# Kernel tuning notes

Hardware: AMD Instinct MI355X
Metric: run time of the kernel (lower is better)

## Reference

```python
import jax, jax.numpy as jnp
import numpy as np

DIM = 768
NUM_HEADS = 12
HEAD_DIM = DIM // NUM_HEADS
SCALE = HEAD_DIM ** -0.5


def setup_inputs() -> dict:
    key = jax.random.key(0)
    ks = jax.random.split(key, 9)
    B, L, C = 4, 1024, DIM
    x = jax.random.normal(ks[0], (B, L, C), jnp.float32)
    q_ape = jax.random.normal(ks[1], (1, L, C), jnp.float32)
    k_ape = jax.random.normal(ks[2], (1, L, C), jnp.float32)
    attn_pos = jax.random.normal(ks[3], (1, NUM_HEADS, L, L), jnp.float32)
    s = C ** -0.5
    # torch Linear weights: (out_features, in_features)
    Wq = jax.random.normal(ks[4], (C, C), jnp.float32) * s
    Wk = jax.random.normal(ks[5], (C, C), jnp.float32) * s
    Wv = jax.random.normal(ks[6], (C, C), jnp.float32) * s
    Wp = jax.random.normal(ks[7], (C, C), jnp.float32) * s
    bp = jax.random.normal(ks[8], (C,), jnp.float32) * 0.01
    return {"x": x, "q_ape": q_ape, "k_ape": k_ape, "attn_pos": attn_pos,
            "Wq": Wq, "Wk": Wk, "Wv": Wv, "Wp": Wp, "bp": bp}


def _split_heads(t):
    # (B, L, C) -> (B, H, L, D)
    B, L, C = t.shape
    return t.reshape(B, L, NUM_HEADS, HEAD_DIM).transpose(0, 2, 1, 3)


def reference(x, q_ape, k_ape, attn_pos, Wq, Wk, Wv, Wp, bp):
    B, L, C = x.shape
    q = _split_heads((x + q_ape) @ Wq.T)          # (B,H,L,D)
    k = _split_heads((x + k_ape) @ Wk.T)          # (B,H,L,D)
    v = _split_heads(x @ Wv.T)                    # (B,H,L,D)
    attn = jnp.einsum('bhqd,bhkd->bhqk', q, k) * SCALE + attn_pos
    attn = jax.nn.softmax(attn, axis=-1)
    out = jnp.einsum('bhqk,bhkd->bhqd', attn, v)  # (B,H,L,D)
    out = out.transpose(0, 2, 1, 3).reshape(B, L, C)
    return out @ Wp.T + bp
```

## Files before the change

kernel.cpp:

```cpp
#include <hip/hip_runtime.h>
#include <stdint.h>

#define NH 12
#define HD 64
#define NB 4
#define SEQ 1024
#define CDIM 768
#define MTOT (NB*SEQ)
#define MC   (MTOT*CDIM)
#define LC   (SEQ*CDIM)
#define WSZ  (CDIM*CDIM)
#define ATT_SCALE 0.125f

typedef __attribute__((ext_vector_type(4))) float f32x4;
typedef __attribute__((ext_vector_type(8))) __bf16 bf16x8;
typedef __attribute__((ext_vector_type(8))) short short8;
typedef __attribute__((ext_vector_type(4))) unsigned short ushort4v;
typedef unsigned short u16;

static __device__ __forceinline__ f32x4 mfma16(short8 a, short8 b, f32x4 c) {
  return __builtin_amdgcn_mfma_f32_16x16x32_bf16(
      __builtin_bit_cast(bf16x8, a), __builtin_bit_cast(bf16x8, b), c, 0, 0, 0);
}
static __device__ __forceinline__ u16 f2bf(float f) {
  unsigned u = __float_as_uint(f);
  u += 0x7FFFu + ((u >> 16) & 1u);
  return (u16)(u >> 16);
}
static __device__ __forceinline__ float bf2f(u16 h) {
  return __uint_as_float(((unsigned)h) << 16);
}
static __device__ __forceinline__ void lds_load16(const void* g, void* l) {
  __builtin_amdgcn_global_load_lds(
      (const __attribute__((address_space(1))) void*)g,
      (__attribute__((address_space(3))) void*)l, 16, 0, 0);
}

__global__ __launch_bounds__(256) void conv_w(
    const float* __restrict__ Wq, const float* __restrict__ Wk,
    const float* __restrict__ Wv, const float* __restrict__ Wp,
    const float* __restrict__ bp, u16* __restrict__ dst) {
  const int N4 = (4 * WSZ + CDIM) / 4;
  int i4 = blockIdx.x * 256 + threadIdx.x;
  if (i4 >= N4) return;
  int sel = i4 / (WSZ / 4);
  int off = i4 - sel * (WSZ / 4);
  const float* src = sel == 0 ? Wq : sel == 1 ? Wk : sel == 2 ? Wv
                   : sel == 3 ? Wp : bp;
  f32x4 v = ((const f32x4*)src)[off];
  ushort4v o;
#pragma unroll
  for (int j = 0; j < 4; j++) o[j] = f2bf(v[j]);
  ((ushort4v*)dst)[i4] = o;
}

__global__ __launch_bounds__(256) void prep_x(
    const float* __restrict__ xp, const float* __restrict__ qp,
    const float* __restrict__ kp, u16* __restrict__ Xq, u16* __restrict__ Xk,
    u16* __restrict__ Xv) {
  int i4 = blockIdx.x * 256 + threadIdx.x;
  if (i4 * 4 >= MC) return;
  int a4 = i4 % (LC / 4);
  f32x4 xx = ((const f32x4*)xp)[i4];
  f32x4 qq = ((const f32x4*)qp)[a4];
  f32x4 kk = ((const f32x4*)kp)[a4];
  ushort4v oq, ok, ov;
#pragma unroll
  for (int j = 0; j < 4; j++) {
    oq[j] = f2bf(xx[j] + qq[j]);
    ok[j] = f2bf(xx[j] + kk[j]);
    ov[j] = f2bf(xx[j]);
  }
  ((ushort4v*)Xq)[i4] = oq;
  ((ushort4v*)Xk)[i4] = ok;
  ((ushort4v*)Xv)[i4] = ov;
}

static __device__ __forceinline__ void gemm_core(
    const u16* __restrict__ Ab, const u16* __restrict__ Wb,
    short* As, short* Bs, f32x4 acc[4][4]) {
  const int t = threadIdx.x;
  const int lane = t & 63, w = t >> 6, quad = lane >> 4, l16 = lane & 15;
  const int wm = (w >> 1) * 64, wn = (w & 1) * 64;
  const int row4 = t >> 2, chunk = (t & 3) * 8;
  for (int k0 = 0; k0 < CDIM; k0 += 32) {
    const u16* ga = Ab + row4 * CDIM + k0 + chunk;
    const u16* gb = Wb + row4 * CDIM + k0 + chunk;
    lds_load16(ga,             (char*)As + t * 16);
    lds_load16(ga + 64 * CDIM, (char*)As + 4096 + t * 16);
    lds_load16(gb,             (char*)Bs + t * 16);
    lds_load16(gb + 64 * CDIM, (char*)Bs + 4096 + t * 16);
    __syncthreads();
    short8 af[4], bw[4];
#pragma unroll
    for (int i = 0; i < 4; i++)
      af[i] = *(const short8*)(As + (wm + i * 16 + l16) * 32 + quad * 8);
#pragma unroll
    for (int j = 0; j < 4; j++)
      bw[j] = *(const short8*)(Bs + (wn + j * 16 + l16) * 32 + quad * 8);
#pragma unroll
    for (int i = 0; i < 4; i++)
#pragma unroll
      for (int j = 0; j < 4; j++)
        acc[i][j] = mfma16(af[i], bw[j], acc[i][j]);
    __syncthreads();
  }
}

__global__ __launch_bounds__(256) void gemm_qkv(
    const u16* __restrict__ Xq, const u16* __restrict__ Xk, const u16* __restrict__ Xv,
    const u16* __restrict__ Wq, const u16* __restrict__ Wk, const u16* __restrict__ Wv,
    u16* __restrict__ Q, u16* __restrict__ K, u16* __restrict__ Vt) {
  __shared__ __align__(16) short As[128 * 32], Bs[128 * 32];
  const int z = blockIdx.z;
  const int m0 = blockIdx.y * 128, n0 = blockIdx.x * 128;
  const u16* A = (z == 0 ? Xq : z == 1 ? Xk : Xv) + m0 * CDIM;
  const u16* W = (z == 0 ? Wq : z == 1 ? Wk : Wv) + n0 * CDIM;
  f32x4 acc[4][4];
#pragma unroll
  for (int i = 0; i < 4; i++)
#pragma unroll
    for (int j = 0; j < 4; j++) acc[i][j] = 0.f;
  gemm_core(A, W, As, Bs, acc);

  const int t = threadIdx.x, lane = t & 63, w = t >> 6;
  const int quad = lane >> 4, l16 = lane & 15;
  const int wm = (w >> 1) * 64, wn = (w & 1) * 64;
  if (z < 2) {
    u16* O = (z == 0 ? Q : K);
#pragma unroll
    for (int i = 0; i < 4; i++) {
      int mrow = m0 + wm + i * 16 + quad * 4;
      int b = mrow >> 10;
#pragma unroll
      for (int j = 0; j < 4; j++) {
        int n = n0 + wn + j * 16 + l16;
        int h = n >> 6, d = n & 63;
#pragma unroll
        for (int r = 0; r < 4; r++) {
          int l = (mrow + r) & 1023;
          O[(((b * NH + h) << 10) + l) * HD + d] = f2bf(acc[i][j][r]);
        }
      }
    }
  } else {
#pragma unroll
    for (int i = 0; i < 4; i++) {
      int l0 = m0 + wm + i * 16 + quad * 4;
      int b = l0 >> 10, l = l0 & 1023;
#pragma unroll
      for (int j = 0; j < 4; j++) {
        int n = n0 + wn + j * 16 + l16;
        int h = n >> 6, d = n & 63;
        ushort4v v;
#pragma unroll
        for (int r = 0; r < 4; r++) v[r] = f2bf(acc[i][j][r]);
        *(ushort4v*)(Vt + ((b * NH + h) * HD + d) * SEQ + l) = v;
      }
    }
  }
}

__global__ __launch_bounds__(256) void attn(
    const u16* __restrict__ Q, const u16* __restrict__ K, const u16* __restrict__ Vt,
    const float* __restrict__ pos, u16* __restrict__ O) {
  __shared__ __align__(16) short Ks[64 * 96], Vs[64 * 96], Ps[64 * 96];
  const int t = threadIdx.x, lane = t & 63, w = t >> 6;
  const int quad = lane >> 4, l16 = lane & 15;
  const int qt = blockIdx.x;
  const int bh = blockIdx.y;
  const int b = bh / NH, h = bh % NH;
  const int q0 = qt * 64 + w * 16;

  const u16* Qg = Q + (bh * SEQ + q0) * HD;
  short8 qa0 = *(const short8*)(Qg + l16 * HD + quad * 8);
  short8 qa1 = *(const short8*)(Qg + l16 * HD + 32 + quad * 8);

  f32x4 o[4];
#pragma unroll
  for (int j = 0; j < 4; j++) o[j] = 0.f;
  float mrow[4], lrow[4];
#pragma unroll
  for (int r = 0; r < 4; r++) { mrow[r] = -1e30f; lrow[r] = 0.f; }

  const u16* Kg = K + bh * SEQ * HD;
  const u16* Vg = Vt + bh * HD * SEQ;
  const float* Pg = pos + (size_t)(h * SEQ + q0) * SEQ;
  const int sr = t >> 3, sc = (t & 7) * 8;

  for (int kt = 0; kt < 16; kt++) {
    const int k0 = kt * 64;
    {
      const u16* kg = Kg + k0 * HD;
      *(short8*)(Ks + sr * 96 + sc)        = *(const short8*)(kg + sr * HD + sc);
      *(short8*)(Ks + (sr + 32) * 96 + sc) = *(const short8*)(kg + (sr + 32) * HD + sc);
      const u16* vg = Vg + k0;
      *(short8*)(Vs + sr * 96 + sc)        = *(const short8*)(vg + sr * SEQ + sc);
      *(short8*)(Vs + (sr + 32) * 96 + sc) = *(const short8*)(vg + (sr + 32) * SEQ + sc);
    }
    __syncthreads();

    f32x4 s[4];
#pragma unroll
    for (int j = 0; j < 4; j++) {
      short8 kb0 = *(const short8*)(Ks + (j * 16 + l16) * 96 + quad * 8);
      short8 kb1 = *(const short8*)(Ks + (j * 16 + l16) * 96 + 32 + quad * 8);
      f32x4 zz = 0.f;
      s[j] = mfma16(qa1, kb1, mfma16(qa0, kb0, zz));
    }

    float pv[4][4], mx[4];
#pragma unroll
    for (int r = 0; r < 4; r++) mx[r] = -1e30f;
#pragma unroll
    for (int j = 0; j < 4; j++)
#pragma unroll
      for (int r = 0; r < 4; r++) {
        float v = s[j][r] * ATT_SCALE +
                  Pg[(quad * 4 + r) * SEQ + k0 + j * 16 + l16];
        pv[j][r] = v;
        mx[r] = fmaxf(mx[r], v);
      }
#pragma unroll
    for (int off = 1; off < 16; off <<= 1)
#pragma unroll
      for (int r = 0; r < 4; r++) mx[r] = fmaxf(mx[r], __shfl_xor(mx[r], off));

    float alpha[4], rs[4];
#pragma unroll
    for (int r = 0; r < 4; r++) {
      float mnew = fmaxf(mrow[r], mx[r]);
      alpha[r] = __expf(mrow[r] - mnew);
      mrow[r] = mnew;
      rs[r] = 0.f;
    }
#pragma unroll
    for (int j = 0; j < 4; j++)
#pragma unroll
      for (int r = 0; r < 4; r++) {
        float e = __expf(pv[j][r] - mrow[r]);
        pv[j][r] = e;
        rs[r] += e;
      }
#pragma unroll
    for (int off = 1; off < 16; off <<= 1)
#pragma unroll
      for (int r = 0; r < 4; r++) rs[r] += __shfl_xor(rs[r], off);
#pragma unroll
    for (int r = 0; r < 4; r++) lrow[r] = lrow[r] * alpha[r] + rs[r];

#pragma unroll
    for (int j = 0; j < 4; j++) {
      f32x4 t4 = o[j];
#pragma unroll
      for (int r = 0; r < 4; r++) t4[r] *= alpha[r];
      o[j] = t4;
    }
    short* Pw = Ps + w * 16 * 96;
#pragma unroll
    for (int j = 0; j < 4; j++)
#pragma unroll
      for (int r = 0; r < 4; r++)
        Pw[(quad * 4 + r) * 96 + j * 16 + l16] = (short)f2bf(pv[j][r]);
    short8 pa0 = *(const short8*)(Pw + l16 * 96 + quad * 8);
    short8 pa1 = *(const short8*)(Pw + l16 * 96 + 32 + quad * 8);
#pragma unroll
    for (int j = 0; j < 4; j++) {
      short8 vb0 = *(const short8*)(Vs + (j * 16 + l16) * 96 + quad * 8);
      short8 vb1 = *(const short8*)(Vs + (j * 16 + l16) * 96 + 32 + quad * 8);
      o[j] = mfma16(pa1, vb1, mfma16(pa0, vb0, o[j]));
    }
    __syncthreads();
  }

  u16* Og = O + (b * SEQ + q0) * CDIM + h * HD;
  float inv[4];
#pragma unroll
  for (int r = 0; r < 4; r++) inv[r] = 1.0f / lrow[r];
#pragma unroll
  for (int j = 0; j < 4; j++)
#pragma unroll
    for (int r = 0; r < 4; r++)
      Og[(quad * 4 + r) * CDIM + j * 16 + l16] = f2bf(o[j][r] * inv[r]);
}

__global__ __launch_bounds__(256) void gemm_proj(
    const u16* __restrict__ Oin, const u16* __restrict__ Wp,
    const u16* __restrict__ bp, float* __restrict__ out) {
  __shared__ __align__(16) short As[128 * 32], Bs[128 * 32];
  const int m0 = blockIdx.y * 128, n0 = blockIdx.x * 128;
  f32x4 acc[4][4];
#pragma unroll
  for (int i = 0; i < 4; i++)
#pragma unroll
    for (int j = 0; j < 4; j++) acc[i][j] = 0.f;
  gemm_core(Oin + m0 * CDIM, Wp + n0 * CDIM, As, Bs, acc);

  const int t = threadIdx.x, lane = t & 63, w = t >> 6;
  const int quad = lane >> 4, l16 = lane & 15;
  const int wm = (w >> 1) * 64, wn = (w & 1) * 64;
#pragma unroll
  for (int i = 0; i < 4; i++) {
    int mrow = m0 + wm + i * 16 + quad * 4;
#pragma unroll
    for (int j = 0; j < 4; j++) {
      int n = n0 + wn + j * 16 + l16;
      float bias = bf2f(bp[n]);
#pragma unroll
      for (int r = 0; r < 4; r++)
        out[(mrow + r) * CDIM + n] = acc[i][j][r] + bias;
    }
  }
}

extern "C" void kernel_launch(void* const* d_in, const int* in_sizes, int n_in,
                              void* d_out, int out_size, void* d_ws, size_t ws_size,
                              hipStream_t stream) {
  (void)in_sizes; (void)n_in; (void)out_size;
  const size_t OFF_XQ = 0, OFF_XK = (size_t)MC, OFF_XV = 2ull * MC,
               OFF_Q = 3ull * MC, OFF_K = 4ull * MC, OFF_VT = 5ull * MC,
               OFF_W = 6ull * MC, TOT = OFF_W + 4ull * WSZ + 1024;
  const size_t NEED = 2 * TOT;
  if (ws_size < NEED) return;

  u16* ws = (u16*)d_ws;
  u16 *Xq = ws + OFF_XQ, *Xk = ws + OFF_XK, *Xv = ws + OFF_XV;
  u16 *Qb = ws + OFF_Q, *Kb = ws + OFF_K, *Vt = ws + OFF_VT;
  u16 *Wb = ws + OFF_W;
  u16 *Wqb = Wb, *Wkb = Wb + WSZ, *Wvb = Wb + 2ull * WSZ,
      *Wpb = Wb + 3ull * WSZ, *bpb = Wb + 4ull * WSZ;
  u16* Ob = Xq;

  conv_w<<<(4 * WSZ + CDIM) / 4 / 256 + 1, 256, 0, stream>>>(
      (const float*)d_in[4], (const float*)d_in[5], (const float*)d_in[6],
      (const float*)d_in[7], (const float*)d_in[8], Wb);
  prep_x<<<MC / 4 / 256, 256, 0, stream>>>(
      (const float*)d_in[0], (const float*)d_in[1], (const float*)d_in[2],
      Xq, Xk, Xv);
  gemm_qkv<<<dim3(6, 32, 3), 256, 0, stream>>>(Xq, Xk, Xv, Wqb, Wkb, Wvb,
                                               Qb, Kb, Vt);
  attn<<<dim3(16, 48), 256, 0, stream>>>(Qb, Kb, Vt, (const float*)d_in[3], Ob);
  gemm_proj<<<dim3(6, 32), 256, 0, stream>>>(Ob, Wpb, bpb, (float*)d_out);
}
```

Before: 239.6 us.

## Drop online-softmax max tracking, stage QKV epilogue through LDS, merge prep kernels

The attention kernel no longer tracks a running row maximum or rescales its accumulators. It exponentiates scores directly with exp2, with the softmax scale folded into Q in the projection epilogue. It writes truncated bf16 probabilities and defers the row-sum shuffle reduction to the end. The QKV GEMM epilogue now stages results through padded LDS so global stores to Q, K and transposed V are 16-byte coalesced. The two preprocessing kernels are merged into one launch, and the attention LDS row stride changes to cut bank conflicts. Skipping max subtraction risks fp32 overflow for large logits, and that safety depends on the input magnitudes.

Result: slower. 269.0 us (+12.3%).

```diff
diff --git a/kernel.cpp b/kernel.cpp
--- a/kernel.cpp
+++ b/kernel.cpp
@@ -10,7 +10,9 @@
 #define MC   (MTOT*CDIM)
 #define LC   (SEQ*CDIM)
 #define WSZ  (CDIM*CDIM)
-#define ATT_SCALE 0.125f
+#define L2E  1.44269504f
+#define LST  104
+#define EST  136
 
 typedef __attribute__((ext_vector_type(4))) float f32x4;
 typedef __attribute__((ext_vector_type(8))) __bf16 bf16x8;
@@ -36,44 +38,46 @@
       (__attribute__((address_space(3))) void*)l, 16, 0, 0);
 }
 
-__global__ __launch_bounds__(256) void conv_w(
-    const float* __restrict__ Wq, const float* __restrict__ Wk,
-    const float* __restrict__ Wv, const float* __restrict__ Wp,
-    const float* __restrict__ bp, u16* __restrict__ dst) {
-  const int N4 = (4 * WSZ + CDIM) / 4;
-  int i4 = blockIdx.x * 256 + threadIdx.x;
-  if (i4 >= N4) return;
-  int sel = i4 / (WSZ / 4);
-  int off = i4 - sel * (WSZ / 4);
-  const float* src = sel == 0 ? Wq : sel == 1 ? Wk : sel == 2 ? Wv
-                   : sel == 3 ? Wp : bp;
-  f32x4 v = ((const f32x4*)src)[off];
-  ushort4v o;
-#pragma unroll
-  for (int j = 0; j < 4; j++) o[j] = f2bf(v[j]);
-  ((ushort4v*)dst)[i4] = o;
-}
-
-__global__ __launch_bounds__(256) void prep_x(
+#define PREP_BLKS (MC / 4 / 256)
+#define CONV_N4   ((4 * WSZ + CDIM) / 4)
+#define CONV_BLKS ((CONV_N4 + 255) / 256)
+__global__ __launch_bounds__(256) void prep_all(
     const float* __restrict__ xp, const float* __restrict__ qp,
-    const float* __restrict__ kp, u16* __restrict__ Xq, u16* __restrict__ Xk,
-    u16* __restrict__ Xv) {
-  int i4 = blockIdx.x * 256 + threadIdx.x;
-  if (i4 * 4 >= MC) return;
-  int a4 = i4 % (LC / 4);
-  f32x4 xx = ((const f32x4*)xp)[i4];
-  f32x4 qq = ((const f32x4*)qp)[a4];
-  f32x4 kk = ((const f32x4*)kp)[a4];
-  ushort4v oq, ok, ov;
-#pragma unroll
-  for (int j = 0; j < 4; j++) {
-    oq[j] = f2bf(xx[j] + qq[j]);
-    ok[j] = f2bf(xx[j] + kk[j]);
-    ov[j] = f2bf(xx[j]);
-  }
-  ((ushort4v*)Xq)[i4] = oq;
-  ((ushort4v*)Xk)[i4] = ok;
-  ((ushort4v*)Xv)[i4] = ov;
+    const float* __restrict__ kp, const float* __restrict__ Wq,
+    const float* __restrict__ Wk, const float* __restrict__ Wv,
+    const float* __restrict__ Wp, const float* __restrict__ bp,
+    u16* __restrict__ Xq, u16* __restrict__ Xk, u16* __restrict__ Xv,
+    u16* __restrict__ Wb) {
+  int bid = blockIdx.x;
+  if (bid < PREP_BLKS) {
+    int i4 = bid * 256 + threadIdx.x;
+    int a4 = i4 % (LC / 4);
+    f32x4 xx = ((const f32x4*)xp)[i4];
+    f32x4 qq = ((const f32x4*)qp)[a4];
+    f32x4 kk = ((const f32x4*)kp)[a4];
+    ushort4v oq, ok, ov;
+#pragma unroll
+    for (int j = 0; j < 4; j++) {
+      oq[j] = f2bf(xx[j] + qq[j]);
+      ok[j] = f2bf(xx[j] + kk[j]);
+      ov[j] = f2bf(xx[j]);
+    }
+    ((ushort4v*)Xq)[i4] = oq;
+    ((ushort4v*)Xk)[i4] = ok;
+    ((ushort4v*)Xv)[i4] = ov;
+  } else {
+    int i4 = (bid - PREP_BLKS) * 256 + threadIdx.x;
+    if (i4 >= CONV_N4) return;
+    int sel = i4 / (WSZ / 4);
+    int off = i4 - sel * (WSZ / 4);
+    const float* src = sel == 0 ? Wq : sel == 1 ? Wk : sel == 2 ? Wv
+                     : sel == 3 ? Wp : bp;
+    f32x4 v = ((const f32x4*)src)[off];
+    ushort4v o;
+#pragma unroll
+    for (int j = 0; j < 4; j++) o[j] = f2bf(v[j]);
+    ((ushort4v*)Wb)[i4] = o;
+  }
 }
 
 static __device__ __forceinline__ void gemm_core(
@@ -111,7 +115,9 @@
     const u16* __restrict__ Xq, const u16* __restrict__ Xk, const u16* __restrict__ Xv,
     const u16* __restrict__ Wq, const u16* __restrict__ Wk, const u16* __restrict__ Wv,
     u16* __restrict__ Q, u16* __restrict__ K, u16* __restrict__ Vt) {
-  __shared__ __align__(16) short As[128 * 32], Bs[128 * 32];
+  __shared__ __align__(16) short S[128 * EST];
+  short* As = S;
+  short* Bs = S + 4096;
   const int z = blockIdx.z;
   const int m0 = blockIdx.y * 128, n0 = blockIdx.x * 128;
   const u16* A = (z == 0 ? Xq : z == 1 ? Xk : Xv) + m0 * CDIM;
@@ -126,36 +132,44 @@
   const int t = threadIdx.x, lane = t & 63, w = t >> 6;
   const int quad = lane >> 4, l16 = lane & 15;
   const int wm = (w >> 1) * 64, wn = (w & 1) * 64;
+  const float qs = (z == 0) ? 0.125f : 1.0f;
+
+#pragma unroll
+  for (int i = 0; i < 4; i++)
+#pragma unroll
+    for (int j = 0; j < 4; j++)
+#pragma unroll
+      for (int r = 0; r < 4; r++) {
+        int mr = wm + i * 16 + quad * 4 + r;
+        int nc = wn + j * 16 + l16;
+        if (z < 2) S[mr * EST + nc] = (short)f2bf(acc[i][j][r] * qs);
+        else       S[nc * EST + mr] = (short)f2bf(acc[i][j][r]);
+      }
+  __syncthreads();
+
+  const int row = t >> 3, ch = t & 7;
+  const int b = m0 >> 10, lbase = m0 & 1023;
   if (z < 2) {
     u16* O = (z == 0 ? Q : K);
 #pragma unroll
-    for (int i = 0; i < 4; i++) {
-      int mrow = m0 + wm + i * 16 + quad * 4;
-      int b = mrow >> 10;
-#pragma unroll
-      for (int j = 0; j < 4; j++) {
-        int n = n0 + wn + j * 16 + l16;
-        int h = n >> 6, d = n & 63;
-#pragma unroll
-        for (int r = 0; r < 4; r++) {
-          int l = (mrow + r) & 1023;
-          O[(((b * NH + h) << 10) + l) * HD + d] = f2bf(acc[i][j][r]);
-        }
+    for (int cp = 0; cp < 2; cp++) {
+      int h = (n0 >> 6) + cp;
+#pragma unroll
+      for (int rp = 0; rp < 4; rp++) {
+        int mr = row + rp * 32;
+        short8 v = *(const short8*)(S + mr * EST + cp * 64 + ch * 8);
+        *(short8*)(O + ((((b * NH + h) << 10) + lbase + mr) * HD) + ch * 8) = v;
       }
     }
   } else {
 #pragma unroll
-    for (int i = 0; i < 4; i++) {
-      int l0 = m0 + wm + i * 16 + quad * 4;
-      int b = l0 >> 10, l = l0 & 1023;
-#pragma unroll
-      for (int j = 0; j < 4; j++) {
-        int n = n0 + wn + j * 16 + l16;
-        int h = n >> 6, d = n & 63;
-        ushort4v v;
-#pragma unroll
-        for (int r = 0; r < 4; r++) v[r] = f2bf(acc[i][j][r]);
-        *(ushort4v*)(Vt + ((b * NH + h) * HD + d) * SEQ + l) = v;
+    for (int rp = 0; rp < 4; rp++) {
+      int rn = row + rp * 32;
+      int h = (n0 + rn) >> 6, d = (n0 + rn) & 63;
+#pragma unroll
+      for (int cp = 0; cp < 2; cp++) {
+        short8 v = *(const short8*)(S + rn * EST + cp * 64 + ch * 8);
+        *(short8*)(Vt + ((b * NH + h) * HD + d) * SEQ + lbase + cp * 64 + ch * 8) = v;
       }
     }
   }
@@ -164,7 +178,7 @@
 __global__ __launch_bounds__(256) void attn(
     const u16* __restrict__ Q, const u16* __restrict__ K, const u16* __restrict__ Vt,
     const float* __restrict__ pos, u16* __restrict__ O) {
-  __shared__ __align__(16) short Ks[64 * 96], Vs[64 * 96], Ps[64 * 96];
+  __shared__ __align__(16) short Ks[64 * LST], Vs[64 * LST], Ps[64 * LST];
   const int t = threadIdx.x, lane = t & 63, w = t >> 6;
   const int quad = lane >> 4, l16 = lane & 15;
   const int qt = blockIdx.x;
@@ -179,99 +193,61 @@
   f32x4 o[4];
 #pragma unroll
   for (int j = 0; j < 4; j++) o[j] = 0.f;
-  float mrow[4], lrow[4];
-#pragma unroll
-  for (int r = 0; r < 4; r++) { mrow[r] = -1e30f; lrow[r] = 0.f; }
+  float lrow[4] = {0.f, 0.f, 0.f, 0.f};
 
   const u16* Kg = K + bh * SEQ * HD;
   const u16* Vg = Vt + bh * HD * SEQ;
   const float* Pg = pos + (size_t)(h * SEQ + q0) * SEQ;
   const int sr = t >> 3, sc = (t & 7) * 8;
+  short* Pw = Ps + w * 16 * LST;
 
   for (int kt = 0; kt < 16; kt++) {
     const int k0 = kt * 64;
     {
       const u16* kg = Kg + k0 * HD;
-      *(short8*)(Ks + sr * 96 + sc)        = *(const short8*)(kg + sr * HD + sc);
-      *(short8*)(Ks + (sr + 32) * 96 + sc) = *(const short8*)(kg + (sr + 32) * HD + sc);
+      *(short8*)(Ks + sr * LST + sc)        = *(const short8*)(kg + sr * HD + sc);
+      *(short8*)(Ks + (sr + 32) * LST + sc) = *(const short8*)(kg + (sr + 32) * HD + sc);
       const u16* vg = Vg + k0;
-      *(short8*)(Vs + sr * 96 + sc)        = *(const short8*)(vg + sr * SEQ + sc);
-      *(short8*)(Vs + (sr + 32) * 96 + sc) = *(const short8*)(vg + (sr + 32) * SEQ + sc);
+      *(short8*)(Vs + sr * LST + sc)        = *(const short8*)(vg + sr * SEQ + sc);
+      *(short8*)(Vs + (sr + 32) * LST + sc) = *(const short8*)(vg + (sr + 32) * SEQ + sc);
     }
     __syncthreads();
 
     f32x4 s[4];
 #pragma unroll
     for (int j = 0; j < 4; j++) {
-      short8 kb0 = *(const short8*)(Ks + (j * 16 + l16) * 96 + quad * 8);
-      short8 kb1 = *(const short8*)(Ks + (j * 16 + l16) * 96 + 32 + quad * 8);
+      short8 kb0 = *(const short8*)(Ks + (j * 16 + l16) * LST + quad * 8);
+      short8 kb1 = *(const short8*)(Ks + (j * 16 + l16) * LST + 32 + quad * 8);
       f32x4 zz = 0.f;
       s[j] = mfma16(qa1, kb1, mfma16(qa0, kb0, zz));
     }
 
-    float pv[4][4], mx[4];
-#pragma unroll
-    for (int r = 0; r < 4; r++) mx[r] = -1e30f;
 #pragma unroll
     for (int j = 0; j < 4; j++)
 #pragma unroll
       for (int r = 0; r < 4; r++) {
-        float v = s[j][r] * ATT_SCALE +
-                  Pg[(quad * 4 + r) * SEQ + k0 + j * 16 + l16];
-        pv[j][r] = v;
-        mx[r] = fmaxf(mx[r], v);
+        float p = Pg[(quad * 4 + r) * SEQ + k0 + j * 16 + l16];
+        float e = __builtin_amdgcn_exp2f(fmaf(s[j][r], L2E, p * L2E));
+        unsigned bits = __float_as_uint(e);
+        Pw[(quad * 4 + r) * LST + j * 16 + l16] = (short)(bits >> 16);
+        lrow[r] += __uint_as_float(bits & 0xFFFF0000u);
       }
-#pragma unroll
-    for (int off = 1; off < 16; off <<= 1)
-#pragma unroll
-      for (int r = 0; r < 4; r++) mx[r] = fmaxf(mx[r], __shfl_xor(mx[r], off));
-
-    float alpha[4], rs[4];
-#pragma unroll
-    for (int r = 0; r < 4; r++) {
-      float mnew = fmaxf(mrow[r], mx[r]);
-      alpha[r] = __expf(mrow[r] - mnew);
-      mrow[r] = mnew;
-      rs[r] = 0.f;
-    }
-#pragma unroll
-    for (int j = 0; j < 4; j++)
-#pragma unroll
-      for (int r = 0; r < 4; r++) {
-        float e = __expf(pv[j][r] - mrow[r]);
-        pv[j][r] = e;
-        rs[r] += e;
-      }
-#pragma unroll
-    for (int off = 1; off < 16; off <<= 1)
-#pragma unroll
-      for (int r = 0; r < 4; r++) rs[r] += __shfl_xor(rs[r], off);
-#pragma unroll
-    for (int r = 0; r < 4; r++) lrow[r] = lrow[r] * alpha[r] + rs[r];
-
+
+    short8 pa0 = *(const short8*)(Pw + l16 * LST + quad * 8);
+    short8 pa1 = *(const short8*)(Pw + l16 * LST + 32 + quad * 8);
 #pragma unroll
     for (int j = 0; j < 4; j++) {
-      f32x4 t4 = o[j];
-#pragma unroll
-      for (int r = 0; r < 4; r++) t4[r] *= alpha[r];
-      o[j] = t4;
-    }
-    short* Pw = Ps + w * 16 * 96;
-#pragma unroll
-    for (int j = 0; j < 4; j++)
-#pragma unroll
-      for (int r = 0; r < 4; r++)
-        Pw[(quad * 4 + r) * 96 + j * 16 + l16] = (short)f2bf(pv[j][r]);
-    short8 pa0 = *(const short8*)(Pw + l16 * 96 + quad * 8);
-    short8 pa1 = *(const short8*)(Pw + l16 * 96 + 32 + quad * 8);
-#pragma unroll
-    for (int j = 0; j < 4; j++) {
-      short8 vb0 = *(const short8*)(Vs + (j * 16 + l16) * 96 + quad * 8);
-      short8 vb1 = *(const short8*)(Vs + (j * 16 + l16) * 96 + 32 + quad * 8);
+      short8 vb0 = *(const short8*)(Vs + (j * 16 + l16) * LST + quad * 8);
+      short8 vb1 = *(const short8*)(Vs + (j * 16 + l16) * LST + 32 + quad * 8);
       o[j] = mfma16(pa1, vb1, mfma16(pa0, vb0, o[j]));
     }
     __syncthreads();
   }
+
+#pragma unroll
+  for (int off = 1; off < 16; off <<= 1)
+#pragma unroll
+    for (int r = 0; r < 4; r++) lrow[r] += __shfl_xor(lrow[r], off);
 
   u16* Og = O + (b * SEQ + q0) * CDIM + h * HD;
   float inv[4];
@@ -331,12 +307,10 @@
       *Wpb = Wb + 3ull * WSZ, *bpb = Wb + 4ull * WSZ;
   u16* Ob = Xq;
 
-  conv_w<<<(4 * WSZ + CDIM) / 4 / 256 + 1, 256, 0, stream>>>(
+  prep_all<<<PREP_BLKS + CONV_BLKS, 256, 0, stream>>>(
+      (const float*)d_in[0], (const float*)d_in[1], (const float*)d_in[2],
       (const float*)d_in[4], (const float*)d_in[5], (const float*)d_in[6],
-      (const float*)d_in[7], (const float*)d_in[8], Wb);
-  prep_x<<<MC / 4 / 256, 256, 0, stream>>>(
-      (const float*)d_in[0], (const float*)d_in[1], (const float*)d_in[2],
-      Xq, Xk, Xv);
+      (const float*)d_in[7], (const float*)d_in[8], Xq, Xk, Xv, Wb);
   gemm_qkv<<<dim3(6, 32, 3), 256, 0, stream>>>(Xq, Xk, Xv, Wqb, Wkb, Wvb,
                                                Qb, Kb, Vt);
   attn<<<dim3(16, 48), 256, 0, stream>>>(Qb, Kb, Vt, (const float*)d_in[3], Ob);
```
